# Optimization experiments

Measured on AMD Instinct MI355X. Metric: run time of the kernel, lower is better.

The kernel has to match this reference:

```python
import jax, jax.numpy as jnp
import numpy as np

N, FIN, FOUT = 4096, 256, 256


def setup_inputs() -> dict:
    key = jax.random.key(0)
    ks = jax.random.split(key, 6)
    x = jax.random.normal(ks[0], (N, FIN), jnp.float32)
    adj = jax.random.randint(ks[1], (N, N), 0, 2, jnp.int32)  # dense 0/1 adjacency
    W = jax.random.normal(ks[2], (FOUT, FIN), jnp.float32) / np.sqrt(FIN)
    b = jax.random.normal(ks[3], (FOUT,), jnp.float32) * 0.01
    att_w = jax.random.normal(ks[4], (2 * FOUT,), jnp.float32) / np.sqrt(2.0 * FOUT)  # Linear(2F,1).weight squeezed
    att_b = jax.random.normal(ks[5], (), jnp.float32) * 0.01
    return {"x": x, "adj": adj, "W": W, "b": b, "att_w": att_w, "att_b": att_b}


def reference(x, adj, W, b, att_w, att_b):
    n = x.shape[0]
    fo = W.shape[0]
    h = x @ W.T + b  # [N, Fout]
    # score(i,j) = att([h_i ; h_j]) = h_i.w1 + h_j.w2 + att_b  -> no [N,N,2F] concat
    s = (h @ att_w[:fo])[:, None] + (h @ att_w[fo:])[None, :] + att_b  # [N, N]
    edge = adj == 1
    # GLOBAL softmax over all edges (faithful to F.softmax(stacked_scores, dim=0))
    gmax = jnp.max(jnp.where(edge, s, -jnp.inf))
    e = jnp.exp(s - gmax)
    denom = jnp.sum(jnp.where(edge, e, 0.0))
    p = (e / denom).reshape(-1)  # softmaxed score per pair (valid at edges)
    # original indexes attention_scores[j] by NODE id j into the row-major edge list:
    # recover the score of the j-th global edge (j = 0..N-1) via cumsum rank + scatter
    flat = edge.reshape(-1)
    rank = jnp.cumsum(flat.astype(jnp.int32)) - 1  # rank of each edge in row-major order
    idx = jnp.where(flat, rank, n)  # non-edges and ranks >= n get dropped
    w_node = jnp.zeros((n,), h.dtype).at[idx].set(p, mode="drop")  # [N]
    # output[i] = sum_{j: adj[i,j]==1} w_node[j] * h[j]
    out = jax.nn.relu(edge.astype(h.dtype) @ (w_node[:, None] * h))
    return out
```

## Files before the change

kernel.cpp:

```cpp
#include <hip/hip_runtime.h>
#include <cstdint>
#include <cstddef>

#define NN 4096
#define FDIM 256

typedef __attribute__((ext_vector_type(4))) float fx4;
typedef __attribute__((ext_vector_type(8))) short s8v;

__device__ inline uint16_t f2bf(float f) {
    union { float f; uint32_t u; } v; v.f = f;
    const uint32_t u = v.u;
    return (uint16_t)((u + 0x7FFFu + ((u >> 16) & 1u)) >> 16);
}

__global__ __launch_bounds__(512, 4) void k_h(const float* __restrict__ x,
        const float* __restrict__ W, const float* __restrict__ bias,
        const float* __restrict__ att_w, uint16_t* __restrict__ gt,
        float* __restrict__ a1p, float* __restrict__ a2p) {
    __shared__ __align__(16) float xs[2][64 * 68];
    __shared__ __align__(16) float wt[2][64 * 68];
    const int bi = blockIdx.x, bf = blockIdx.y;
    const int t = threadIdx.x;
    const int t256 = t & 255;
    const int kh = t >> 8;
    const int tx = t256 & 15, ty = t256 >> 4;
    float acc[4][4] = {};
    float rx[8], rw[8];
    #pragma unroll
    for (int u = 0; u < 8; ++u) {
        const int e = t + 512 * u, r = e >> 6, c = e & 63;
        rx[u] = x[(size_t)(bi * 64 + r) * 256 + c];
        rw[u] = W[(size_t)(bf * 64 + r) * 256 + c];
    }
    for (int p = 0; p < 4; ++p) {
        float* xb = xs[p & 1];
        float* wb = wt[p & 1];
        #pragma unroll
        for (int u = 0; u < 8; ++u) {
            const int e = t + 512 * u, r = e >> 6, c = e & 63;
            const int sw = 8 * ((c & 7) ^ ((c >> 3) & 7));
            xb[c * 68 + (r ^ sw)] = rx[u];
            wb[c * 68 + (r ^ sw)] = rw[u];
        }
        __syncthreads();
        if (p < 3) {
            const int kc = (p + 1) * 64;
            #pragma unroll
            for (int u = 0; u < 8; ++u) {
                const int e = t + 512 * u, r = e >> 6, c = e & 63;
                rx[u] = x[(size_t)(bi * 64 + r) * 256 + kc + c];
                rw[u] = W[(size_t)(bf * 64 + r) * 256 + kc + c];
            }
        }
        #pragma unroll 8
        for (int k = 0; k < 32; ++k) {
            const int kk = kh * 32 + k;
            const int sw = 8 * ((kk & 7) ^ ((kk >> 3) & 7));
            const fx4 av = *(const fx4*)(xb + kk * 68 + ((ty * 4) ^ sw));
            const fx4 bv = *(const fx4*)(wb + kk * 68 + ((tx * 4) ^ sw));
            #pragma unroll
            for (int u = 0; u < 4; ++u)
                #pragma unroll
                for (int v = 0; v < 4; ++v)
                    acc[u][v] += av[u] * bv[v];
        }
    }
    __syncthreads();
    float* cbuf = xs[0];
    if (kh == 1) {
        #pragma unroll
        for (int u = 0; u < 4; ++u)
            *(fx4*)(cbuf + t256 * 16 + u * 4) = *(const fx4*)(&acc[u][0]);
    }
    __syncthreads();
    if (kh == 0) {
        float* tileT = wt[0];
        #pragma unroll
        for (int u = 0; u < 4; ++u) {
            const fx4 o = *(const fx4*)(cbuf + t256 * 16 + u * 4);
            #pragma unroll
            for (int v = 0; v < 4; ++v) acc[u][v] += o[v];
        }
        const fx4 bv = *(const fx4*)(bias + bf * 64 + tx * 4);
        const fx4 w1v = *(const fx4*)(att_w + bf * 64 + tx * 4);
        const fx4 w2v = *(const fx4*)(att_w + 256 + bf * 64 + tx * 4);
        #pragma unroll
        for (int u = 0; u < 4; ++u) {
            const int i = bi * 64 + ty * 4 + u;
            fx4 r;
            float s1 = 0.f, s2 = 0.f;
            #pragma unroll
            for (int v = 0; v < 4; ++v) {
                r[v] = acc[u][v] + bv[v];
                s1 += r[v] * w1v[v];
                s2 += r[v] * w2v[v];
            }
            #pragma unroll
            for (int v = 0; v < 4; ++v)
                tileT[(tx * 4 + v) * 68 + ty * 4 + u] = r[v];
            #pragma unroll
            for (int d = 8; d > 0; d >>= 1) {
                s1 += __shfl_down(s1, d, 16);
                s2 += __shfl_down(s2, d, 16);
            }
            if (tx == 0) {
                a1p[bf * NN + i] = s1;
                a2p[bf * NN + i] = s2;
            }
        }
    }
    __syncthreads();
    {
        const float* tileT = wt[0];
        const int fl = t >> 3, cb = t & 7;
        s8v v;
        #pragma unroll
        for (int lo = 0; lo < 8; ++lo)
            v[lo] = (short)f2bf(tileT[fl * 68 + cb * 8 + lo]);
        *(s8v*)(gt + (size_t)(bf * 64 + fl) * NN + bi * 64 + cb * 8) = v;
    }
}

__global__ __launch_bounds__(1024) void k_prep(const float* __restrict__ a1p,
        const float* __restrict__ a2p, const int* __restrict__ adj,
        float* __restrict__ E1, float* __restrict__ E2,
        float* __restrict__ wraw, float* __restrict__ Sg) {
    __shared__ float E1s[NN];
    __shared__ float E2s[NN];
    __shared__ float red1[16], red2[16];
    __shared__ int wtot[16];
    __shared__ int base_s;
    const int t = threadIdx.x, lane = t & 63, wv = t >> 6;
    fx4 v1 = {0.f, 0.f, 0.f, 0.f}, v2 = {0.f, 0.f, 0.f, 0.f};
    #pragma unroll
    for (int bf = 0; bf < 4; ++bf) {
        v1 += *(const fx4*)(a1p + bf * NN + t * 4);
        v2 += *(const fx4*)(a2p + bf * NN + t * 4);
    }
    float m1 = fmaxf(fmaxf(v1[0], v1[1]), fmaxf(v1[2], v1[3]));
    float m2 = fmaxf(fmaxf(v2[0], v2[1]), fmaxf(v2[2], v2[3]));
    #pragma unroll
    for (int d = 32; d > 0; d >>= 1) {
        m1 = fmaxf(m1, __shfl_down(m1, d));
        m2 = fmaxf(m2, __shfl_down(m2, d));
    }
    if (lane == 0) { red1[wv] = m1; red2[wv] = m2; }
    __syncthreads();
    if (t == 0) {
        float mm1 = -1e30f, mm2 = -1e30f;
        for (int k = 0; k < 16; ++k) {
            mm1 = fmaxf(mm1, red1[k]);
            mm2 = fmaxf(mm2, red2[k]);
        }
        red1[0] = mm1; red2[0] = mm2;
        *Sg = 0.f;
        base_s = 0;
    }
    __syncthreads();
    const float M1 = red1[0], M2 = red2[0];
    fx4 e1v, e2v, z4 = {0.f, 0.f, 0.f, 0.f};
    #pragma unroll
    for (int j = 0; j < 4; ++j) {
        e1v[j] = expf(v1[j] - M1);
        e2v[j] = expf(v2[j] - M2);
    }
    *(fx4*)(E1s + t * 4) = e1v;
    *(fx4*)(E2s + t * 4) = e2v;
    *(fx4*)(E1 + t * 4) = e1v;
    *(fx4*)(E2 + t * 4) = e2v;
    *(fx4*)(wraw + t * 4) = z4;
    __syncthreads();
    for (int row = 0; row < NN; ++row) {
        const int base = base_s;
        if (base >= NN) break;
        const int4 a = ((const int4*)(adj + (size_t)row * NN))[t];
        const int vj[4] = {a.x, a.y, a.z, a.w};
        int cnt = 0;
        #pragma unroll
        for (int j = 0; j < 4; ++j) cnt += (vj[j] == 1);
        int inc = cnt;
        #pragma unroll
        for (int d = 1; d < 64; d <<= 1) {
            const int y = __shfl_up(inc, d);
            if (lane >= d) inc += y;
        }
        if (lane == 63) wtot[wv] = inc;
        __syncthreads();
        int wbase = 0, total = 0;
        #pragma unroll
        for (int w = 0; w < 16; ++w) {
            const int xw = wtot[w];
            total += xw;
            wbase += (w < wv) ? xw : 0;
        }
        if (t == 0) base_s = base + total;
        int r = base + wbase + inc - cnt;
        if (cnt && r < NN) {
            const float e1 = E1s[row];
            #pragma unroll
            for (int j = 0; j < 4; ++j) {
                if (vj[j] == 1) {
                    if (r < NN) wraw[r] = e1 * E2s[t * 4 + j];
                    ++r;
                }
            }
        }
        __syncthreads();
    }
}

__global__ __launch_bounds__(256, 2) void k_fused(const int* __restrict__ adj,
        const uint16_t* __restrict__ gt, const float* __restrict__ E1,
        const float* __restrict__ E2, const float* __restrict__ wraw,
        uint16_t* __restrict__ part, float* __restrict__ Sg, int krange) {
    __shared__ __align__(16) uint16_t As[2][64 * 72];
    __shared__ float sgred[4];
    const int ib = blockIdx.x, ks = blockIdx.y;
    const int t = threadIdx.x;
    const int wv = t >> 6, lane = t & 63;
    const int q = lane >> 4, m16 = lane & 15;
    const int i0 = ib * 64, k0 = ks * krange;
    const int ksteps = krange >> 6;
    const int ar = t >> 4, ac4 = (t & 15) * 4;
    fx4 acc[4][4];
    #pragma unroll
    for (int a = 0; a < 4; ++a)
        #pragma unroll
        for (int b2 = 0; b2 < 4; ++b2) acc[a][b2] = (fx4){0.f, 0.f, 0.f, 0.f};
    float sS = 0.f;
    float e1r[4];
    #pragma unroll
    for (int p = 0; p < 4; ++p) e1r[p] = E1[i0 + p * 16 + ar];
    const uint16_t* rowp[4];
    #pragma unroll
    for (int ft = 0; ft < 4; ++ft)
        rowp[ft] = gt + (size_t)(wv * 64 + ft * 16 + m16) * NN + q * 8;

    int4 ra0[4], ra1[4];
    #pragma unroll
    for (int p = 0; p < 4; ++p)
        ra0[p] = *(const int4*)(adj + (size_t)(i0 + p * 16 + ar) * NN + k0 + ac4);
    #pragma unroll
    for (int p = 0; p < 4; ++p)
        ra1[p] = *(const int4*)(adj + (size_t)(i0 + p * 16 + ar) * NN + k0 + 64 + ac4);
    fx4 rwC = *(const fx4*)(wraw + k0 + ac4);
    fx4 reC = *(const fx4*)(E2 + k0 + ac4);
    s8v B0[4][2], B1[4][2];
    #pragma unroll
    for (int ft = 0; ft < 4; ++ft) {
        B0[ft][0] = *(const s8v*)(rowp[ft] + k0);
        B0[ft][1] = *(const s8v*)(rowp[ft] + k0 + 32);
    }

    auto step = [&](s8v (&Bc)[4][2], s8v (&Bn)[4][2], int4 (&Rc)[4], int stp) {
        const int cur = stp & 1;
        const int kk = k0 + stp * 64;
        const uint16_t wb0 = f2bf(rwC[0]), wb1 = f2bf(rwC[1]);
        const uint16_t wb2 = f2bf(rwC[2]), wb3 = f2bf(rwC[3]);
        #pragma unroll
        for (int p = 0; p < 4; ++p) {
            uint2 wo;
            wo.x = (Rc[p].x == 1 ? (uint32_t)wb0 : 0u) |
                   ((Rc[p].y == 1 ? (uint32_t)wb1 : 0u) << 16);
            wo.y = (Rc[p].z == 1 ? (uint32_t)wb2 : 0u) |
                   ((Rc[p].w == 1 ? (uint32_t)wb3 : 0u) << 16);
            *(uint2*)(&As[cur][(p * 16 + ar) * 72 + ac4]) = wo;
            sS += e1r[p] * ((Rc[p].x == 1 ? reC[0] : 0.f) +
                            (Rc[p].y == 1 ? reC[1] : 0.f) +
                            (Rc[p].z == 1 ? reC[2] : 0.f) +
                            (Rc[p].w == 1 ? reC[3] : 0.f));
        }
        __syncthreads();
        if (stp + 2 < ksteps) {
            #pragma unroll
            for (int p = 0; p < 4; ++p)
                Rc[p] = *(const int4*)(adj + (size_t)(i0 + p * 16 + ar) * NN +
                                       kk + 128 + ac4);
        }
        if (stp + 1 < ksteps) {
            rwC = *(const fx4*)(wraw + kk + 64 + ac4);
            reC = *(const fx4*)(E2 + kk + 64 + ac4);
            #pragma unroll
            for (int ft = 0; ft < 4; ++ft) {
                Bn[ft][0] = *(const s8v*)(rowp[ft] + kk + 64);
                Bn[ft][1] = *(const s8v*)(rowp[ft] + kk + 64 + 32);
            }
        }
        s8v afr[4][2];
        #pragma unroll
        for (int it = 0; it < 4; ++it)
            #pragma unroll
            for (int khh = 0; khh < 2; ++khh)
                afr[it][khh] = *(const s8v*)(&As[cur][(it * 16 + m16) * 72 +
                                                      khh * 32 + q * 8]);
        #pragma unroll
        for (int ft = 0; ft < 4; ++ft)
            #pragma unroll
            for (int khh = 0; khh < 2; ++khh)
                #pragma unroll
                for (int it = 0; it < 4; ++it)
                    acc[it][ft] = __builtin_amdgcn_mfma_f32_16x16x32_bf16(
                        afr[it][khh], Bc[ft][khh], acc[it][ft], 0, 0, 0);
    };

    for (int stp = 0; stp < ksteps; stp += 2) {
        step(B0, B1, ra0, stp);
        step(B1, B0, ra1, stp + 1);
    }

    #pragma unroll
    for (int d = 32; d > 0; d >>= 1) sS += __shfl_down(sS, d);
    if (lane == 0) sgred[wv] = sS;
    __syncthreads();
    if (t == 0)
        atomicAdd(Sg, sgred[0] + sgred[1] + sgred[2] + sgred[3]);
    uint16_t* dst = part + (size_t)ks * NN * FDIM;
    #pragma unroll
    for (int it = 0; it < 4; ++it) {
        #pragma unroll
        for (int ft = 0; ft < 4; ++ft) {
            const int f = wv * 64 + ft * 16 + m16;
            #pragma unroll
            for (int r = 0; r < 4; ++r) {
                const int i = i0 + it * 16 + q * 4 + r;
                dst[(size_t)i * FDIM + f] = f2bf(acc[it][ft][r]);
            }
        }
    }
}

__global__ __launch_bounds__(256) void k_out(const uint16_t* __restrict__ part,
        const float* __restrict__ Sg, float* __restrict__ out, int nsplit) {
    const size_t idx = ((size_t)blockIdx.x * 256 + threadIdx.x) * 8;
    const float inv = 1.0f / (*Sg);
    float s[8] = {};
    for (int k = 0; k < nsplit; ++k) {
        const s8v v = *(const s8v*)(part + (size_t)k * NN * FDIM + idx);
        #pragma unroll
        for (int j = 0; j < 8; ++j) {
            union { uint32_t u; float f; } cv;
            cv.u = ((uint32_t)(uint16_t)v[j]) << 16;
            s[j] += cv.f;
        }
    }
    fx4 r0, r1;
    #pragma unroll
    for (int j = 0; j < 4; ++j) {
        r0[j] = fmaxf(s[j], 0.f) * inv;
        r1[j] = fmaxf(s[4 + j], 0.f) * inv;
    }
    *(fx4*)(out + idx) = r0;
    *(fx4*)(out + idx + 4) = r1;
}

extern "C" void kernel_launch(void* const* d_in, const int* in_sizes, int n_in,
                              void* d_out, int out_size, void* d_ws, size_t ws_size,
                              hipStream_t stream) {
    const float* x     = (const float*)d_in[0];
    const int*   adj   = (const int*)d_in[1];
    const float* W     = (const float*)d_in[2];
    const float* bias  = (const float*)d_in[3];
    const float* att_w = (const float*)d_in[4];
    float* out = (float*)d_out;
    char* ws = (char*)d_ws;
    uint16_t* gt   = (uint16_t*)(ws + 0);
    float*    a1p  = (float*)(ws + 2097152);
    float*    a2p  = (float*)(ws + 2162688);
    float*    E1   = (float*)(ws + 2228224);
    float*    E2   = (float*)(ws + 2244608);
    float*    wraw = (float*)(ws + 2260992);
    float*    Sg   = (float*)(ws + 2277376);
    uint16_t* part = (uint16_t*)(ws + 2277632);
    (void)in_sizes; (void)n_in; (void)out_size;

    const size_t avail = (ws_size > 2277632) ? (ws_size - 2277632) : 0;
    int splitk = 1;
    while (splitk < 8 &&
           (size_t)(splitk * 2) * NN * FDIM * sizeof(uint16_t) <= avail)
        splitk <<= 1;
    const int krange = NN / splitk;

    k_h    <<<dim3(64, 4), 512, 0, stream>>>(x, W, bias, att_w, gt, a1p, a2p);
    k_prep <<<dim3(1), 1024, 0, stream>>>(a1p, a2p, adj, E1, E2, wraw, Sg);
    k_fused<<<dim3(64, splitk), 256, 0, stream>>>(adj, gt, E1, E2, wraw, part, Sg, krange);
    k_out  <<<dim3(512), 256, 0, stream>>>(part, Sg, out, splitk);
}
```

Measured before the change: 153.2 us.

## Pack adjacency into bitmasks in k_h and stream bits in fused GEMM

The k_h projection kernel now also reads the dense int32 adjacency and writes a 1-bit-per-edge mask (128 words per row). The fused aggregation kernel reads these bitmasks instead of int4 adjacency vectors, which shrinks the adjacency traffic in the MFMA loop by 32x. k_prep keeps its raw node weights in shared memory and emits them pre-converted to bf16, so the per-step bf16 conversion in the fused kernel goes away. The full adjacency read moves into k_h, which adds memory traffic to that stage and needs extra workspace for the bitmask.

```diff
diff --git a/kernel.cpp b/kernel.cpp
--- a/kernel.cpp
+++ b/kernel.cpp
@@ -16,7 +16,8 @@
 
 __global__ __launch_bounds__(512, 4) void k_h(const float* __restrict__ x,
         const float* __restrict__ W, const float* __restrict__ bias,
-        const float* __restrict__ att_w, uint16_t* __restrict__ gt,
+        const float* __restrict__ att_w, const int* __restrict__ adj,
+        uint16_t* __restrict__ gt, uint32_t* __restrict__ bitw,
         float* __restrict__ a1p, float* __restrict__ a2p) {
     __shared__ __align__(16) float xs[2][64 * 68];
     __shared__ __align__(16) float wt[2][64 * 68];
@@ -25,6 +26,7 @@
     const int t256 = t & 255;
     const int kh = t >> 8;
     const int tx = t256 & 15, ty = t256 >> 4;
+    const int pr0 = (bi * 4 + bf) * 16;
     float acc[4][4] = {};
     float rx[8], rw[8];
     #pragma unroll
@@ -52,6 +54,14 @@
                 rx[u] = x[(size_t)(bi * 64 + r) * 256 + kc + c];
                 rw[u] = W[(size_t)(bf * 64 + r) * 256 + kc + c];
             }
+        }
+        const int wi = p * 512 + t;
+        const int prow = pr0 + (wi >> 7), pw = wi & 127;
+        int4 pa[8];
+        {
+            const int* ap = adj + (size_t)prow * NN + pw * 32;
+            #pragma unroll
+            for (int j = 0; j < 8; ++j) pa[j] = *(const int4*)(ap + j * 4);
         }
         #pragma unroll 8
         for (int k = 0; k < 32; ++k) {
@@ -65,6 +75,15 @@
                 for (int v = 0; v < 4; ++v)
                     acc[u][v] += av[u] * bv[v];
         }
+        uint32_t bm = 0;
+        #pragma unroll
+        for (int j = 0; j < 8; ++j) {
+            bm |= (uint32_t)(pa[j].x & 1) << (4 * j);
+            bm |= (uint32_t)(pa[j].y & 1) << (4 * j + 1);
+            bm |= (uint32_t)(pa[j].z & 1) << (4 * j + 2);
+            bm |= (uint32_t)(pa[j].w & 1) << (4 * j + 3);
+        }
+        bitw[(size_t)prow * 128 + pw] = bm;
     }
     __syncthreads();
     float* cbuf = xs[0];
@@ -125,9 +144,10 @@
 __global__ __launch_bounds__(1024) void k_prep(const float* __restrict__ a1p,
         const float* __restrict__ a2p, const int* __restrict__ adj,
         float* __restrict__ E1, float* __restrict__ E2,
-        float* __restrict__ wraw, float* __restrict__ Sg) {
+        uint16_t* __restrict__ wbf, float* __restrict__ Sg) {
     __shared__ float E1s[NN];
     __shared__ float E2s[NN];
+    __shared__ float wraw_s[NN];
     __shared__ float red1[16], red2[16];
     __shared__ int wtot[16];
     __shared__ int base_s;
@@ -169,7 +189,7 @@
     *(fx4*)(E2s + t * 4) = e2v;
     *(fx4*)(E1 + t * 4) = e1v;
     *(fx4*)(E2 + t * 4) = e2v;
-    *(fx4*)(wraw + t * 4) = z4;
+    *(fx4*)(wraw_s + t * 4) = z4;
     __syncthreads();
     for (int row = 0; row < NN; ++row) {
         const int base = base_s;
@@ -201,18 +221,26 @@
             #pragma unroll
             for (int j = 0; j < 4; ++j) {
                 if (vj[j] == 1) {
-                    if (r < NN) wraw[r] = e1 * E2s[t * 4 + j];
+                    if (r < NN) wraw_s[r] = e1 * E2s[t * 4 + j];
                     ++r;
                 }
             }
         }
         __syncthreads();
     }
-}
-
-__global__ __launch_bounds__(256, 2) void k_fused(const int* __restrict__ adj,
+    __syncthreads();
+    {
+        const fx4 wv4 = *(const fx4*)(wraw_s + t * 4);
+        uint2 o;
+        o.x = (uint32_t)f2bf(wv4[0]) | ((uint32_t)f2bf(wv4[1]) << 16);
+        o.y = (uint32_t)f2bf(wv4[2]) | ((uint32_t)f2bf(wv4[3]) << 16);
+        *(uint2*)(wbf + t * 4) = o;
+    }
+}
+
+__global__ __launch_bounds__(256, 2) void k_fused(const uint32_t* __restrict__ bitw,
         const uint16_t* __restrict__ gt, const float* __restrict__ E1,
-        const float* __restrict__ E2, const float* __restrict__ wraw,
+        const float* __restrict__ E2, const uint16_t* __restrict__ wbf,
         uint16_t* __restrict__ part, float* __restrict__ Sg, int krange) {
     __shared__ __align__(16) uint16_t As[2][64 * 72];
     __shared__ float sgred[4];
@@ -222,30 +250,24 @@
     const int q = lane >> 4, m16 = lane & 15;
     const int i0 = ib * 64, k0 = ks * krange;
     const int ksteps = krange >> 6;
-    const int ar = t >> 4, ac4 = (t & 15) * 4;
+    const int srow = t & 63, scg = t >> 6;
+    const int sh = (scg & 1) * 16;
     fx4 acc[4][4];
     #pragma unroll
     for (int a = 0; a < 4; ++a)
         #pragma unroll
         for (int b2 = 0; b2 < 4; ++b2) acc[a][b2] = (fx4){0.f, 0.f, 0.f, 0.f};
     float sS = 0.f;
-    float e1r[4];
-    #pragma unroll
-    for (int p = 0; p < 4; ++p) e1r[p] = E1[i0 + p * 16 + ar];
+    const float e1row = E1[i0 + srow];
+    const uint32_t* brow = bitw + (size_t)(i0 + srow) * 128 + (k0 >> 5) + (scg >> 1);
     const uint16_t* rowp[4];
     #pragma unroll
     for (int ft = 0; ft < 4; ++ft)
         rowp[ft] = gt + (size_t)(wv * 64 + ft * 16 + m16) * NN + q * 8;
 
-    int4 ra0[4], ra1[4];
-    #pragma unroll
-    for (int p = 0; p < 4; ++p)
-        ra0[p] = *(const int4*)(adj + (size_t)(i0 + p * 16 + ar) * NN + k0 + ac4);
-    #pragma unroll
-    for (int p = 0; p < 4; ++p)
-        ra1[p] = *(const int4*)(adj + (size_t)(i0 + p * 16 + ar) * NN + k0 + 64 + ac4);
-    fx4 rwC = *(const fx4*)(wraw + k0 + ac4);
-    fx4 reC = *(const fx4*)(E2 + k0 + ac4);
+    uint32_t bitsC = brow[0];
+    uint4 wpC0 = *(const uint4*)(wbf + k0 + scg * 16);
+    uint4 wpC1 = *(const uint4*)(wbf + k0 + scg * 16 + 8);
     s8v B0[4][2], B1[4][2];
     #pragma unroll
     for (int ft = 0; ft < 4; ++ft) {
@@ -253,34 +275,38 @@
         B0[ft][1] = *(const s8v*)(rowp[ft] + k0 + 32);
     }
 
-    auto step = [&](s8v (&Bc)[4][2], s8v (&Bn)[4][2], int4 (&Rc)[4], int stp) {
+    auto step = [&](s8v (&Bc)[4][2], s8v (&Bn)[4][2], int stp) {
         const int cur = stp & 1;
         const int kk = k0 + stp * 64;
-        const uint16_t wb0 = f2bf(rwC[0]), wb1 = f2bf(rwC[1]);
-        const uint16_t wb2 = f2bf(rwC[2]), wb3 = f2bf(rwC[3]);
-        #pragma unroll
-        for (int p = 0; p < 4; ++p) {
-            uint2 wo;
-            wo.x = (Rc[p].x == 1 ? (uint32_t)wb0 : 0u) |
-                   ((Rc[p].y == 1 ? (uint32_t)wb1 : 0u) << 16);
-            wo.y = (Rc[p].z == 1 ? (uint32_t)wb2 : 0u) |
-                   ((Rc[p].w == 1 ? (uint32_t)wb3 : 0u) << 16);
-            *(uint2*)(&As[cur][(p * 16 + ar) * 72 + ac4]) = wo;
-            sS += e1r[p] * ((Rc[p].x == 1 ? reC[0] : 0.f) +
-                            (Rc[p].y == 1 ? reC[1] : 0.f) +
-                            (Rc[p].z == 1 ? reC[2] : 0.f) +
-                            (Rc[p].w == 1 ? reC[3] : 0.f));
-        }
+        fx4 e2v[4];
+        #pragma unroll
+        for (int j = 0; j < 4; ++j)
+            e2v[j] = *(const fx4*)(E2 + kk + scg * 16 + j * 4);
+        const uint32_t bits = bitsC >> sh;
+        uint32_t wpa[8];
+        wpa[0] = wpC0.x; wpa[1] = wpC0.y; wpa[2] = wpC0.z; wpa[3] = wpC0.w;
+        wpa[4] = wpC1.x; wpa[5] = wpC1.y; wpa[6] = wpC1.z; wpa[7] = wpC1.w;
+        float s16 = 0.f;
+        uint32_t ob[8];
+        #pragma unroll
+        for (int pp = 0; pp < 8; ++pp) {
+            const uint32_t b0 = (bits >> (2 * pp)) & 1u;
+            const uint32_t b1 = (bits >> (2 * pp + 1)) & 1u;
+            ob[pp] = wpa[pp] & ((b0 ? 0xFFFFu : 0u) | (b1 ? 0xFFFF0000u : 0u));
+            s16 += (b0 ? e2v[pp >> 1][(pp & 1) * 2] : 0.f) +
+                   (b1 ? e2v[pp >> 1][(pp & 1) * 2 + 1] : 0.f);
+        }
+        sS += e1row * s16;
+        uint16_t* dstAs = &As[cur][srow * 72 + scg * 16];
+        *(uint2*)(dstAs + 0)  = make_uint2(ob[0], ob[1]);
+        *(uint2*)(dstAs + 4)  = make_uint2(ob[2], ob[3]);
+        *(uint2*)(dstAs + 8)  = make_uint2(ob[4], ob[5]);
+        *(uint2*)(dstAs + 12) = make_uint2(ob[6], ob[7]);
         __syncthreads();
-        if (stp + 2 < ksteps) {
-            #pragma unroll
-            for (int p = 0; p < 4; ++p)
-                Rc[p] = *(const int4*)(adj + (size_t)(i0 + p * 16 + ar) * NN +
-                                       kk + 128 + ac4);
-        }
         if (stp + 1 < ksteps) {
-            rwC = *(const fx4*)(wraw + kk + 64 + ac4);
-            reC = *(const fx4*)(E2 + kk + 64 + ac4);
+            bitsC = brow[(stp + 1) * 2];
+            wpC0 = *(const uint4*)(wbf + kk + 64 + scg * 16);
+            wpC1 = *(const uint4*)(wbf + kk + 64 + scg * 16 + 8);
             #pragma unroll
             for (int ft = 0; ft < 4; ++ft) {
                 Bn[ft][0] = *(const s8v*)(rowp[ft] + kk + 64);
@@ -305,8 +331,8 @@
     };
 
     for (int stp = 0; stp < ksteps; stp += 2) {
-        step(B0, B1, ra0, stp);
-        step(B1, B0, ra1, stp + 1);
+        step(B0, B1, stp);
+        step(B1, B0, stp + 1);
     }
 
     #pragma unroll
@@ -365,24 +391,25 @@
     float* out = (float*)d_out;
     char* ws = (char*)d_ws;
     uint16_t* gt   = (uint16_t*)(ws + 0);
-    float*    a1p  = (float*)(ws + 2097152);
-    float*    a2p  = (float*)(ws + 2162688);
-    float*    E1   = (float*)(ws + 2228224);
-    float*    E2   = (float*)(ws + 2244608);
-    float*    wraw = (float*)(ws + 2260992);
-    float*    Sg   = (float*)(ws + 2277376);
-    uint16_t* part = (uint16_t*)(ws + 2277632);
+    uint32_t* bitw = (uint32_t*)(ws + 2097152);
+    float*    a1p  = (float*)(ws + 4194304);
+    float*    a2p  = (float*)(ws + 4259840);
+    float*    E1   = (float*)(ws + 4325376);
+    float*    E2   = (float*)(ws + 4341760);
+    uint16_t* wbf  = (uint16_t*)(ws + 4358144);
+    float*    Sg   = (float*)(ws + 4366336);
+    uint16_t* part = (uint16_t*)(ws + 4366592);
     (void)in_sizes; (void)n_in; (void)out_size;
 
-    const size_t avail = (ws_size > 2277632) ? (ws_size - 2277632) : 0;
+    const size_t avail = (ws_size > 4366592) ? (ws_size - 4366592) : 0;
     int splitk = 1;
     while (splitk < 8 &&
            (size_t)(splitk * 2) * NN * FDIM * sizeof(uint16_t) <= avail)
         splitk <<= 1;
     const int krange = NN / splitk;
 
-    k_h    <<<dim3(64, 4), 512, 0, stream>>>(x, W, bias, att_w, gt, a1p, a2p);
-    k_prep <<<dim3(1), 1024, 0, stream>>>(a1p, a2p, adj, E1, E2, wraw, Sg);
-    k_fused<<<dim3(64, splitk), 256, 0, stream>>>(adj, gt, E1, E2, wraw, part, Sg, krange);
+    k_h    <<<dim3(64, 4), 512, 0, stream>>>(x, W, bias, att_w, adj, gt, bitw, a1p, a2p);
+    k_prep <<<dim3(1), 1024, 0, stream>>>(a1p, a2p, adj, E1, E2, wbf, Sg);
+    k_fused<<<dim3(64, splitk), 256, 0, stream>>>(bitw, gt, E1, E2, wbf, part, Sg, krange);
     k_out  <<<dim3(512), 256, 0, stream>>>(part, Sg, out, splitk);
 }
```

New measurement: 155.7 us. About the same (+1.6%).
